# Kernel tuning notes

Hardware: AMD Instinct MI355X
Metric: run time of the kernel (lower is better)

Reference implementation:

```python
import jax, jax.numpy as jnp
import numpy as np

N, C_IN, H, W = 64, 8, 256, 256
E = 4      # edge_emb_dim
D = 4      # node_emb_dim
K = 3      # kernel_size
DN = ('NCHW', 'OIHW', 'NCHW')


def conv2d(x, w, b, padding):
    y = jax.lax.conv_general_dilated(x, w, (1, 1), padding, dimension_numbers=DN)
    return y + b[None, :, None, None]


def _w(key, shape):
    fan_in = shape[1] * shape[2] * shape[3]
    return jax.random.normal(key, shape, dtype=jnp.float32) / np.sqrt(fan_in)


def setup_inputs() -> dict:
    key = jax.random.key(0)
    ks = jax.random.split(key, 16)
    return {
        'x': jax.random.normal(ks[0], (N, C_IN, H, W), dtype=jnp.float32),
        # downsampling: 1x1 conv C_IN -> E (kernel=stride=downsampling_factor=1)
        'w_down': _w(ks[1], (E, C_IN, 1, 1)), 'b_down': jnp.zeros((E,), jnp.float32),
        # edge network phi: two conv3x3 (E->E) each followed by silu
        'w_e1': _w(ks[2], (E, E, K, K)), 'b_e1': jnp.zeros((E,), jnp.float32),
        'w_e2': _w(ks[3], (E, E, K, K)), 'b_e2': jnp.zeros((E,), jnp.float32),
        # upsampling: ConvTranspose with kernel=stride=1 == 1x1 conv E -> E
        'w_up': _w(ks[4], (E, E, 1, 1)), 'b_up': jnp.zeros((E,), jnp.float32),
        # node network psi: conv3x3 (C_IN+E -> D), silu, conv3x3 (D -> D)
        'w_n1': _w(ks[5], (D, C_IN + E, K, K)), 'b_n1': jnp.zeros((D,), jnp.float32),
        'w_n2': _w(ks[6], (D, D, K, K)), 'b_n2': jnp.zeros((D,), jnp.float32),
        # pre_resid: 1x1 conv C_IN -> D (since in_channels != node_emb_dim)
        'w_r': _w(ks[7], (D, C_IN, 1, 1)), 'b_r': jnp.zeros((D,), jnp.float32),
    }


def reference(x, w_down, b_down, w_e1, b_e1, w_e2, b_e2, w_up, b_up,
              w_n1, b_n1, w_n2, b_n2, w_r, b_r):
    # vmap(downsampling)(x): treat cell axis N as conv batch. (N,E,H,W)
    z = conv2d(x, w_down, b_down, 'VALID')
    # cell-wise edge CNN phi
    h = jax.nn.silu(conv2d(z, w_e1, b_e1, 'SAME'))
    h = jax.nn.silu(conv2d(h, w_e2, b_e2, 'SAME'))
    # sum-aggregate over cells -> A: (E,H,W)
    A = h.sum(axis=0)
    # upsampling (kernel=stride=1 transpose conv == 1x1 conv); pad is a no-op here
    A = conv2d(A[None], w_up, b_up, 'VALID')[0]
    # node update: concat [x, A] on channels, cell-interaction CNN psi
    y = jnp.concatenate([x, jnp.broadcast_to(A[None], (N, E, H, W))], axis=1)
    y = jax.nn.silu(conv2d(y, w_n1, b_n1, 'SAME'))
    y = conv2d(y, w_n2, b_n2, 'SAME')
    # residual with channel-matching 1x1 conv
    y = y + conv2d(x, w_r, b_r, 'VALID')
    return y
```

## Files before the change

### kernel.cpp

```cpp
#include <hip/hip_runtime.h>
#include <hip/hip_bf16.h>

#define NCELL 64
#define CIN 8
#define EE 4
#define DD 4
#define HH 256
#define WW 256

#define EBH 32
#define NBH 26
#define NBANDS_E (HH / EBH)
#define NBANDS_N ((HH + NBH - 1) / NBH)
#define NSTRIP 5

__device__ __forceinline__ float4 f4z() { return make_float4(0.f, 0.f, 0.f, 0.f); }
__device__ __forceinline__ float silu1(float v) { return v / (1.0f + __expf(-v)); }
__device__ __forceinline__ float4 silu4f(const float a[4]) {
    return make_float4(silu1(a[0]), silu1(a[1]), silu1(a[2]), silu1(a[3]));
}
__device__ __forceinline__ float4 shfL(float4 v) {
    return make_float4(__shfl_up(v.x, 1), __shfl_up(v.y, 1),
                       __shfl_up(v.z, 1), __shfl_up(v.w, 1));
}
__device__ __forceinline__ float4 shfR(float4 v) {
    return make_float4(__shfl_down(v.x, 1), __shfl_down(v.y, 1),
                       __shfl_down(v.z, 1), __shfl_down(v.w, 1));
}

#define COMP(v,i) ((i)==0?(v).x:(i)==1?(v).y:(i)==2?(v).z:(v).w)

__device__ __forceinline__ void conv_group(const float4* L, const float4* C, const float4* R,
                                           const float* __restrict__ w, int ostride, int ibase,
                                           float acc[4]) {
#pragma unroll
    for (int dy = 0; dy < 3; ++dy) {
#pragma unroll
        for (int ci = 0; ci < 4; ++ci) {
            const float aL = COMP(L[dy], ci);
            const float aC = COMP(C[dy], ci);
            const float aR = COMP(R[dy], ci);
#pragma unroll
            for (int o = 0; o < 4; ++o) {
                const int base = o * ostride + (ibase + ci) * 9 + dy * 3;
                acc[o] = fmaf(aL, w[base + 0], acc[o]);
                acc[o] = fmaf(aC, w[base + 1], acc[o]);
                acc[o] = fmaf(aR, w[base + 2], acc[o]);
            }
        }
    }
}

__global__ __launch_bounds__(256) void edge_kernel(
    const float* __restrict__ x,
    const float* __restrict__ w_down, const float* __restrict__ b_down,
    const float* __restrict__ w_e1, const float* __restrict__ b_e1,
    const float* __restrict__ w_e2, const float* __restrict__ b_e2,
    float4* __restrict__ P)
{
    const int lane = threadIdx.x & 63;
    const int wv = threadIdx.x >> 6;
    const int y0 = blockIdx.x * EBH;
    const int s = blockIdx.y;
    const int n = blockIdx.z * 4 + wv;
    const int cx = s * 60 + lane - 2;
    const bool colok = (unsigned)cx < (unsigned)WW;
    const bool payload = (lane >= 2) && (lane < 62) && colok;
    const float* __restrict__ xn = x + (size_t)n * CIN * HH * WW;

    const float bd0 = b_down[0], bd1 = b_down[1], bd2 = b_down[2], bd3 = b_down[3];
    const float be10 = b_e1[0], be11 = b_e1[1], be12 = b_e1[2], be13 = b_e1[3];
    const float be20 = b_e2[0], be21 = b_e2[1], be22 = b_e2[2], be23 = b_e2[3];

    float4 za0 = f4z(), za1 = f4z(), za2 = f4z();
    float4 zb0 = f4z(), zb1 = f4z(), zb2 = f4z();
    float4 zc0 = f4z(), zc1 = f4z(), zc2 = f4z();
    float4 ha0 = f4z(), ha1 = f4z(), ha2 = f4z();
    float4 hb0 = f4z(), hb1 = f4z(), hb2 = f4z();
    float4 hc0 = f4z(), hc1 = f4z(), hc2 = f4z();

    for (int k = 0; k < EBH + 4; ++k) {
        const int zr = y0 - 2 + k;

        float4 zn = f4z();
        if ((unsigned)zr < (unsigned)HH) {
            if (colok) {
                float a0 = bd0, a1 = bd1, a2 = bd2, a3 = bd3;
#pragma unroll
                for (int i = 0; i < CIN; ++i) {
                    const float xv = xn[((size_t)i * HH + zr) * WW + cx];
                    a0 = fmaf(xv, w_down[0 * CIN + i], a0);
                    a1 = fmaf(xv, w_down[1 * CIN + i], a1);
                    a2 = fmaf(xv, w_down[2 * CIN + i], a2);
                    a3 = fmaf(xv, w_down[3 * CIN + i], a3);
                }
                zn = make_float4(a0, a1, a2, a3);
            }
        }
        za0 = za1; za1 = za2; za2 = zn;
        zb0 = zb1; zb1 = zb2; zb2 = shfL(zn);
        zc0 = zc1; zc1 = zc2; zc2 = shfR(zn);

        if (k >= 2) {
            float acc[4] = { be10, be11, be12, be13 };
            {
                float4 L[3] = { zb0, zb1, zb2 };
                float4 C[3] = { za0, za1, za2 };
                float4 R[3] = { zc0, zc1, zc2 };
                conv_group(L, C, R, w_e1, 36, 0, acc);
            }
            const int hr = zr - 1;
            const float4 hn = ((unsigned)hr < (unsigned)HH && colok) ? silu4f(acc) : f4z();
            ha0 = ha1; ha1 = ha2; ha2 = hn;
            hb0 = hb1; hb1 = hb2; hb2 = shfL(hn);
            hc0 = hc1; hc1 = hc2; hc2 = shfR(hn);
        }

        if (k >= 4) {
            float acc[4] = { be20, be21, be22, be23 };
            {
                float4 L[3] = { hb0, hb1, hb2 };
                float4 C[3] = { ha0, ha1, ha2 };
                float4 R[3] = { hc0, hc1, hc2 };
                conv_group(L, C, R, w_e2, 36, 0, acc);
            }
            if (payload) {
                const int orow = zr - 2;
                P[(size_t)n * (HH * WW) + orow * WW + cx] = silu4f(acc);
            }
        }
    }
}

__global__ __launch_bounds__(256) void reduce_kernel(
    const float4* __restrict__ P, float4* __restrict__ A4)
{
    const int p = blockIdx.x * 256 + threadIdx.x;
    float4 a = f4z(), b = f4z(), c = f4z(), d = f4z();
#pragma unroll
    for (int nn = 0; nn < NCELL; nn += 4) {
        const float4 v0 = P[(size_t)(nn + 0) * (HH * WW) + p];
        const float4 v1 = P[(size_t)(nn + 1) * (HH * WW) + p];
        const float4 v2 = P[(size_t)(nn + 2) * (HH * WW) + p];
        const float4 v3 = P[(size_t)(nn + 3) * (HH * WW) + p];
        a.x += v0.x; a.y += v0.y; a.z += v0.z; a.w += v0.w;
        b.x += v1.x; b.y += v1.y; b.z += v1.z; b.w += v1.w;
        c.x += v2.x; c.y += v2.y; c.z += v2.z; c.w += v2.w;
        d.x += v3.x; d.y += v3.y; d.z += v3.z; d.w += v3.w;
    }
    A4[p] = make_float4(a.x + b.x + c.x + d.x, a.y + b.y + c.y + d.y,
                        a.z + b.z + c.z + d.z, a.w + b.w + c.w + d.w);
}

__global__ __launch_bounds__(256) void node_kernel(
    const float* __restrict__ x, const float* __restrict__ A,
    const float* __restrict__ w_up, const float* __restrict__ b_up,
    const float* __restrict__ w_n1, const float* __restrict__ b_n1,
    const float* __restrict__ w_n2, const float* __restrict__ b_n2,
    const float* __restrict__ w_r, const float* __restrict__ b_r,
    float* __restrict__ out)
{
    const int lane = threadIdx.x & 63;
    const int wv = threadIdx.x >> 6;
    const int y0 = blockIdx.x * NBH;
    const int h = min(NBH, HH - y0);
    const int s = blockIdx.y;
    const int n = blockIdx.z * 4 + wv;
    const int cx = s * 60 + lane - 2;
    const bool colok = (unsigned)cx < (unsigned)WW;
    const bool payload = (lane >= 2) && (lane < 62) && colok;
    const float* __restrict__ xn = x + (size_t)n * CIN * HH * WW;
    const float4* __restrict__ A4 = reinterpret_cast<const float4*>(A);

    const float bu0 = b_up[0], bu1 = b_up[1], bu2 = b_up[2], bu3 = b_up[3];
    const float bn10 = b_n1[0], bn11 = b_n1[1], bn12 = b_n1[2], bn13 = b_n1[3];
    const float br0 = b_n2[0] + b_r[0], br1 = b_n2[1] + b_r[1];
    const float br2 = b_n2[2] + b_r[2], br3 = b_n2[3] + b_r[3];

    float4 sa[3][3];
#pragma unroll
    for (int g = 0; g < 3; ++g) { sa[g][0] = f4z(); sa[g][1] = f4z(); sa[g][2] = f4z(); }
    float4 ya[3] = { f4z(), f4z(), f4z() };
    float4 yb[3] = { f4z(), f4z(), f4z() };
    float4 yc[3] = { f4z(), f4z(), f4z() };

    for (int k = 0; k < h + 4; ++k) {
        const int zr = y0 - 2 + k;

        float4 Sn0 = f4z(), Sn1 = f4z(), Sn2 = f4z();
        if ((unsigned)zr < (unsigned)HH) {
            if (colok) {
                float xv[CIN];
#pragma unroll
                for (int i = 0; i < CIN; ++i) xv[i] = xn[((size_t)i * HH + zr) * WW + cx];
                Sn0 = make_float4(xv[0], xv[1], xv[2], xv[3]);
                Sn1 = make_float4(xv[4], xv[5], xv[6], xv[7]);
                const float4 a4 = A4[zr * WW + cx];
                float u0 = bu0, u1 = bu1, u2 = bu2, u3 = bu3;
#pragma unroll
                for (int e = 0; e < 4; ++e) {
                    const float av = COMP(a4, e);
                    u0 = fmaf(av, w_up[0 * EE + e], u0);
                    u1 = fmaf(av, w_up[1 * EE + e], u1);
                    u2 = fmaf(av, w_up[2 * EE + e], u2);
                    u3 = fmaf(av, w_up[3 * EE + e], u3);
                }
                Sn2 = make_float4(u0, u1, u2, u3);
            }
        }
        sa[0][0] = sa[0][1]; sa[0][1] = sa[0][2]; sa[0][2] = Sn0;
        sa[1][0] = sa[1][1]; sa[1][1] = sa[1][2]; sa[1][2] = Sn1;
        sa[2][0] = sa[2][1]; sa[2][1] = sa[2][2]; sa[2][2] = Sn2;

        if (k >= 2) {
            float acc[4] = { bn10, bn11, bn12, bn13 };
#pragma unroll
            for (int g = 0; g < 3; ++g) {
                float4 L[3] = { shfL(sa[g][0]), shfL(sa[g][1]), shfL(sa[g][2]) };
                float4 R[3] = { shfR(sa[g][0]), shfR(sa[g][1]), shfR(sa[g][2]) };
                conv_group(L, sa[g], R, w_n1, 108, 4 * g, acc);
            }
            const int hr = zr - 1;
            const float4 yn = ((unsigned)hr < (unsigned)HH && colok) ? silu4f(acc) : f4z();
            ya[0] = ya[1]; ya[1] = ya[2]; ya[2] = yn;
            yb[0] = yb[1]; yb[1] = yb[2]; yb[2] = shfL(yn);
            yc[0] = yc[1]; yc[1] = yc[2]; yc[2] = shfR(yn);
        }

        if (k >= 4) {
            float acc[4] = { br0, br1, br2, br3 };
            conv_group(yb, ya, yc, w_n2, 36, 0, acc);
#pragma unroll
            for (int g = 0; g < 2; ++g) {
                const float4 xr = (g == 0) ? sa[0][0] : sa[1][0];
#pragma unroll
                for (int ci = 0; ci < 4; ++ci) {
                    const float a = COMP(xr, ci);
                    acc[0] = fmaf(a, w_r[0 * CIN + g * 4 + ci], acc[0]);
                    acc[1] = fmaf(a, w_r[1 * CIN + g * 4 + ci], acc[1]);
                    acc[2] = fmaf(a, w_r[2 * CIN + g * 4 + ci], acc[2]);
                    acc[3] = fmaf(a, w_r[3 * CIN + g * 4 + ci], acc[3]);
                }
            }
            if (payload) {
                const int orow = zr - 2;
#pragma unroll
                for (int o = 0; o < 4; ++o)
                    out[(((size_t)n * DD + o) * HH + orow) * WW + cx] = acc[o];
            }
        }
    }
}

extern "C" void kernel_launch(void* const* d_in, const int* in_sizes, int n_in,
                              void* d_out, int out_size, void* d_ws, size_t ws_size,
                              hipStream_t stream) {
    const float* x      = (const float*)d_in[0];
    const float* w_down = (const float*)d_in[1];
    const float* b_down = (const float*)d_in[2];
    const float* w_e1   = (const float*)d_in[3];
    const float* b_e1   = (const float*)d_in[4];
    const float* w_e2   = (const float*)d_in[5];
    const float* b_e2   = (const float*)d_in[6];
    const float* w_up   = (const float*)d_in[7];
    const float* b_up   = (const float*)d_in[8];
    const float* w_n1   = (const float*)d_in[9];
    const float* b_n1   = (const float*)d_in[10];
    const float* w_n2   = (const float*)d_in[11];
    const float* b_n2   = (const float*)d_in[12];
    const float* w_r    = (const float*)d_in[13];
    const float* b_r    = (const float*)d_in[14];
    float* out = (float*)d_out;

    float4* P = (float4*)d_out;
    float* A  = (float*)d_ws;

    edge_kernel<<<dim3(NBANDS_E, NSTRIP, NCELL / 4), dim3(256), 0, stream>>>(
        x, w_down, b_down, w_e1, b_e1, w_e2, b_e2, P);

    reduce_kernel<<<dim3(HH * WW / 256), dim3(256), 0, stream>>>(P, (float4*)A);

    node_kernel<<<dim3(NBANDS_N, NSTRIP, NCELL / 4), dim3(256), 0, stream>>>(
        x, A, w_up, b_up, w_n1, b_n1, w_n2, b_n2, w_r, b_r, out);
}
```

Measured before the change: 311.5 us.

## Move weights into constant memory, halve band heights, split reduce across cells

A prep kernel repacks all conv weights and biases into a __constant__ buffer laid out as output-channel float4 vectors, so each kernel reads weights with vector constant loads instead of scattered scalar global loads. Row-band heights drop from 32/26 to 16/13, giving more blocks and more parallelism at the cost of more halo recomputation. The reduction kernel now splits the 64-cell sum across four waves and combines them through shared memory, which gives four times more blocks. The change adds an extra kernel launch and a hipGetSymbolAddress call on every invocation.

```diff
diff --git a/kernel.cpp b/kernel.cpp
--- a/kernel.cpp
+++ b/kernel.cpp
@@ -8,16 +8,31 @@
 #define HH 256
 #define WW 256
 
-#define EBH 32
-#define NBH 26
+#define EBH 16
+#define NBH 13
 #define NBANDS_E (HH / EBH)
 #define NBANDS_N ((HH + NBH - 1) / NBH)
 #define NSTRIP 5
 
+#define DOWN4 0
+#define E14   8
+#define E24   44
+#define UP4   80
+#define N14   84
+#define N24   192
+#define R4    228
+#define B4    236
+#define CW4_TOTAL 242
+
+__constant__ __align__(16) float CW[CW4_TOTAL * 4];
+
+#define CWF4(i) (reinterpret_cast<const float4*>(CW)[(i)])
+#define COMP(v,i) ((i)==0?(v).x:(i)==1?(v).y:(i)==2?(v).z:(v).w)
+
 __device__ __forceinline__ float4 f4z() { return make_float4(0.f, 0.f, 0.f, 0.f); }
 __device__ __forceinline__ float silu1(float v) { return v / (1.0f + __expf(-v)); }
-__device__ __forceinline__ float4 silu4f(const float a[4]) {
-    return make_float4(silu1(a[0]), silu1(a[1]), silu1(a[2]), silu1(a[3]));
+__device__ __forceinline__ float4 silu4(float4 v) {
+    return make_float4(silu1(v.x), silu1(v.y), silu1(v.z), silu1(v.w));
 }
 __device__ __forceinline__ float4 shfL(float4 v) {
     return make_float4(__shfl_up(v.x, 1), __shfl_up(v.y, 1),
@@ -27,36 +42,58 @@
     return make_float4(__shfl_down(v.x, 1), __shfl_down(v.y, 1),
                        __shfl_down(v.z, 1), __shfl_down(v.w, 1));
 }
-
-#define COMP(v,i) ((i)==0?(v).x:(i)==1?(v).y:(i)==2?(v).z:(v).w)
+__device__ __forceinline__ void fma4(float4& a, float s, float4 w) {
+    a.x = fmaf(s, w.x, a.x);
+    a.y = fmaf(s, w.y, a.y);
+    a.z = fmaf(s, w.z, a.z);
+    a.w = fmaf(s, w.w, a.w);
+}
 
 __device__ __forceinline__ void conv_group(const float4* L, const float4* C, const float4* R,
-                                           const float* __restrict__ w, int ostride, int ibase,
-                                           float acc[4]) {
+                                           int base4, float4& acc) {
 #pragma unroll
     for (int dy = 0; dy < 3; ++dy) {
 #pragma unroll
         for (int ci = 0; ci < 4; ++ci) {
-            const float aL = COMP(L[dy], ci);
-            const float aC = COMP(C[dy], ci);
-            const float aR = COMP(R[dy], ci);
-#pragma unroll
-            for (int o = 0; o < 4; ++o) {
-                const int base = o * ostride + (ibase + ci) * 9 + dy * 3;
-                acc[o] = fmaf(aL, w[base + 0], acc[o]);
-                acc[o] = fmaf(aC, w[base + 1], acc[o]);
-                acc[o] = fmaf(aR, w[base + 2], acc[o]);
-            }
-        }
+            const int b = base4 + ci * 9 + dy * 3;
+            fma4(acc, COMP(L[dy], ci), CWF4(b + 0));
+            fma4(acc, COMP(C[dy], ci), CWF4(b + 1));
+            fma4(acc, COMP(R[dy], ci), CWF4(b + 2));
+        }
+    }
+}
+
+__global__ __launch_bounds__(128) void prep_kernel(
+    const float* __restrict__ wd, const float* __restrict__ bd,
+    const float* __restrict__ we1, const float* __restrict__ be1,
+    const float* __restrict__ we2, const float* __restrict__ be2,
+    const float* __restrict__ wu, const float* __restrict__ bu,
+    const float* __restrict__ wn1, const float* __restrict__ bn1,
+    const float* __restrict__ wn2, const float* __restrict__ bn2,
+    const float* __restrict__ wr, const float* __restrict__ br,
+    float4* __restrict__ cw)
+{
+    const int t = threadIdx.x;
+    if (t < 8)   cw[DOWN4 + t] = make_float4(wd[t], wd[8 + t], wd[16 + t], wd[24 + t]);
+    if (t < 36)  cw[E14 + t]   = make_float4(we1[t], we1[36 + t], we1[72 + t], we1[108 + t]);
+    if (t < 36)  cw[E24 + t]   = make_float4(we2[t], we2[36 + t], we2[72 + t], we2[108 + t]);
+    if (t < 4)   cw[UP4 + t]   = make_float4(wu[t], wu[4 + t], wu[8 + t], wu[12 + t]);
+    if (t < 108) cw[N14 + t]   = make_float4(wn1[t], wn1[108 + t], wn1[216 + t], wn1[324 + t]);
+    if (t < 36)  cw[N24 + t]   = make_float4(wn2[t], wn2[36 + t], wn2[72 + t], wn2[108 + t]);
+    if (t < 8)   cw[R4 + t]    = make_float4(wr[t], wr[8 + t], wr[16 + t], wr[24 + t]);
+    if (t == 0) {
+        cw[B4 + 0] = make_float4(bd[0], bd[1], bd[2], bd[3]);
+        cw[B4 + 1] = make_float4(be1[0], be1[1], be1[2], be1[3]);
+        cw[B4 + 2] = make_float4(be2[0], be2[1], be2[2], be2[3]);
+        cw[B4 + 3] = make_float4(bu[0], bu[1], bu[2], bu[3]);
+        cw[B4 + 4] = make_float4(bn1[0], bn1[1], bn1[2], bn1[3]);
+        cw[B4 + 5] = make_float4(bn2[0] + br[0], bn2[1] + br[1],
+                                 bn2[2] + br[2], bn2[3] + br[3]);
     }
 }
 
 __global__ __launch_bounds__(256) void edge_kernel(
-    const float* __restrict__ x,
-    const float* __restrict__ w_down, const float* __restrict__ b_down,
-    const float* __restrict__ w_e1, const float* __restrict__ b_e1,
-    const float* __restrict__ w_e2, const float* __restrict__ b_e2,
-    float4* __restrict__ P)
+    const float* __restrict__ x, float4* __restrict__ P)
 {
     const int lane = threadIdx.x & 63;
     const int wv = threadIdx.x >> 6;
@@ -68,9 +105,9 @@
     const bool payload = (lane >= 2) && (lane < 62) && colok;
     const float* __restrict__ xn = x + (size_t)n * CIN * HH * WW;
 
-    const float bd0 = b_down[0], bd1 = b_down[1], bd2 = b_down[2], bd3 = b_down[3];
-    const float be10 = b_e1[0], be11 = b_e1[1], be12 = b_e1[2], be13 = b_e1[3];
-    const float be20 = b_e2[0], be21 = b_e2[1], be22 = b_e2[2], be23 = b_e2[3];
+    const float4 bdn = CWF4(B4 + 0);
+    const float4 be1 = CWF4(B4 + 1);
+    const float4 be2 = CWF4(B4 + 2);
 
     float4 za0 = f4z(), za1 = f4z(), za2 = f4z();
     float4 zb0 = f4z(), zb1 = f4z(), zb2 = f4z();
@@ -83,50 +120,42 @@
         const int zr = y0 - 2 + k;
 
         float4 zn = f4z();
-        if ((unsigned)zr < (unsigned)HH) {
-            if (colok) {
-                float a0 = bd0, a1 = bd1, a2 = bd2, a3 = bd3;
-#pragma unroll
-                for (int i = 0; i < CIN; ++i) {
-                    const float xv = xn[((size_t)i * HH + zr) * WW + cx];
-                    a0 = fmaf(xv, w_down[0 * CIN + i], a0);
-                    a1 = fmaf(xv, w_down[1 * CIN + i], a1);
-                    a2 = fmaf(xv, w_down[2 * CIN + i], a2);
-                    a3 = fmaf(xv, w_down[3 * CIN + i], a3);
-                }
-                zn = make_float4(a0, a1, a2, a3);
-            }
+        if ((unsigned)zr < (unsigned)HH && colok) {
+            zn = bdn;
+#pragma unroll
+            for (int i = 0; i < CIN; ++i)
+                fma4(zn, xn[((size_t)i * HH + zr) * WW + cx], CWF4(DOWN4 + i));
         }
         za0 = za1; za1 = za2; za2 = zn;
         zb0 = zb1; zb1 = zb2; zb2 = shfL(zn);
         zc0 = zc1; zc1 = zc2; zc2 = shfR(zn);
 
         if (k >= 2) {
-            float acc[4] = { be10, be11, be12, be13 };
+            float4 acc = be1;
             {
                 float4 L[3] = { zb0, zb1, zb2 };
                 float4 C[3] = { za0, za1, za2 };
                 float4 R[3] = { zc0, zc1, zc2 };
-                conv_group(L, C, R, w_e1, 36, 0, acc);
+                conv_group(L, C, R, E14, acc);
             }
             const int hr = zr - 1;
-            const float4 hn = ((unsigned)hr < (unsigned)HH && colok) ? silu4f(acc) : f4z();
+            const float4 hn = ((unsigned)hr < (unsigned)HH && colok) ? silu4(acc) : f4z();
             ha0 = ha1; ha1 = ha2; ha2 = hn;
             hb0 = hb1; hb1 = hb2; hb2 = shfL(hn);
             hc0 = hc1; hc1 = hc2; hc2 = shfR(hn);
         }
 
         if (k >= 4) {
-            float acc[4] = { be20, be21, be22, be23 };
+            float4 acc = be2;
             {
                 float4 L[3] = { hb0, hb1, hb2 };
                 float4 C[3] = { ha0, ha1, ha2 };
                 float4 R[3] = { hc0, hc1, hc2 };
-                conv_group(L, C, R, w_e2, 36, 0, acc);
+                conv_group(L, C, R, E24, acc);
             }
             if (payload) {
                 const int orow = zr - 2;
-                P[(size_t)n * (HH * WW) + orow * WW + cx] = silu4f(acc);
+                P[(size_t)n * (HH * WW) + orow * WW + cx] = silu4(acc);
             }
         }
     }
@@ -135,29 +164,30 @@
 __global__ __launch_bounds__(256) void reduce_kernel(
     const float4* __restrict__ P, float4* __restrict__ A4)
 {
-    const int p = blockIdx.x * 256 + threadIdx.x;
-    float4 a = f4z(), b = f4z(), c = f4z(), d = f4z();
-#pragma unroll
-    for (int nn = 0; nn < NCELL; nn += 4) {
-        const float4 v0 = P[(size_t)(nn + 0) * (HH * WW) + p];
-        const float4 v1 = P[(size_t)(nn + 1) * (HH * WW) + p];
-        const float4 v2 = P[(size_t)(nn + 2) * (HH * WW) + p];
-        const float4 v3 = P[(size_t)(nn + 3) * (HH * WW) + p];
+    __shared__ float4 buf[256];
+    const int tid = threadIdx.x;
+    const int pix = blockIdx.x * 64 + (tid & 63);
+    const int c0 = (tid >> 6) * 16;
+    float4 a = f4z(), b = f4z();
+#pragma unroll
+    for (int j = 0; j < 16; j += 2) {
+        const float4 v0 = P[(size_t)(c0 + j + 0) * (HH * WW) + pix];
+        const float4 v1 = P[(size_t)(c0 + j + 1) * (HH * WW) + pix];
         a.x += v0.x; a.y += v0.y; a.z += v0.z; a.w += v0.w;
         b.x += v1.x; b.y += v1.y; b.z += v1.z; b.w += v1.w;
-        c.x += v2.x; c.y += v2.y; c.z += v2.z; c.w += v2.w;
-        d.x += v3.x; d.y += v3.y; d.z += v3.z; d.w += v3.w;
-    }
-    A4[p] = make_float4(a.x + b.x + c.x + d.x, a.y + b.y + c.y + d.y,
-                        a.z + b.z + c.z + d.z, a.w + b.w + c.w + d.w);
+    }
+    buf[tid] = make_float4(a.x + b.x, a.y + b.y, a.z + b.z, a.w + b.w);
+    __syncthreads();
+    if (tid < 64) {
+        const float4 p0 = buf[tid], p1 = buf[tid + 64], p2 = buf[tid + 128], p3 = buf[tid + 192];
+        A4[blockIdx.x * 64 + tid] =
+            make_float4(p0.x + p1.x + p2.x + p3.x, p0.y + p1.y + p2.y + p3.y,
+                        p0.z + p1.z + p2.z + p3.z, p0.w + p1.w + p2.w + p3.w);
+    }
 }
 
 __global__ __launch_bounds__(256) void node_kernel(
     const float* __restrict__ x, const float* __restrict__ A,
-    const float* __restrict__ w_up, const float* __restrict__ b_up,
-    const float* __restrict__ w_n1, const float* __restrict__ b_n1,
-    const float* __restrict__ w_n2, const float* __restrict__ b_n2,
-    const float* __restrict__ w_r, const float* __restrict__ b_r,
     float* __restrict__ out)
 {
     const int lane = threadIdx.x & 63;
@@ -172,10 +202,9 @@
     const float* __restrict__ xn = x + (size_t)n * CIN * HH * WW;
     const float4* __restrict__ A4 = reinterpret_cast<const float4*>(A);
 
-    const float bu0 = b_up[0], bu1 = b_up[1], bu2 = b_up[2], bu3 = b_up[3];
-    const float bn10 = b_n1[0], bn11 = b_n1[1], bn12 = b_n1[2], bn13 = b_n1[3];
-    const float br0 = b_n2[0] + b_r[0], br1 = b_n2[1] + b_r[1];
-    const float br2 = b_n2[2] + b_r[2], br3 = b_n2[3] + b_r[3];
+    const float4 bup = CWF4(B4 + 3);
+    const float4 bn1 = CWF4(B4 + 4);
+    const float4 bn2r = CWF4(B4 + 5);
 
     float4 sa[3][3];
 #pragma unroll
@@ -188,65 +217,51 @@
         const int zr = y0 - 2 + k;
 
         float4 Sn0 = f4z(), Sn1 = f4z(), Sn2 = f4z();
-        if ((unsigned)zr < (unsigned)HH) {
-            if (colok) {
-                float xv[CIN];
-#pragma unroll
-                for (int i = 0; i < CIN; ++i) xv[i] = xn[((size_t)i * HH + zr) * WW + cx];
-                Sn0 = make_float4(xv[0], xv[1], xv[2], xv[3]);
-                Sn1 = make_float4(xv[4], xv[5], xv[6], xv[7]);
-                const float4 a4 = A4[zr * WW + cx];
-                float u0 = bu0, u1 = bu1, u2 = bu2, u3 = bu3;
-#pragma unroll
-                for (int e = 0; e < 4; ++e) {
-                    const float av = COMP(a4, e);
-                    u0 = fmaf(av, w_up[0 * EE + e], u0);
-                    u1 = fmaf(av, w_up[1 * EE + e], u1);
-                    u2 = fmaf(av, w_up[2 * EE + e], u2);
-                    u3 = fmaf(av, w_up[3 * EE + e], u3);
-                }
-                Sn2 = make_float4(u0, u1, u2, u3);
-            }
+        if ((unsigned)zr < (unsigned)HH && colok) {
+            float xv[CIN];
+#pragma unroll
+            for (int i = 0; i < CIN; ++i) xv[i] = xn[((size_t)i * HH + zr) * WW + cx];
+            Sn0 = make_float4(xv[0], xv[1], xv[2], xv[3]);
+            Sn1 = make_float4(xv[4], xv[5], xv[6], xv[7]);
+            const float4 a4 = A4[zr * WW + cx];
+            Sn2 = bup;
+#pragma unroll
+            for (int e = 0; e < 4; ++e)
+                fma4(Sn2, COMP(a4, e), CWF4(UP4 + e));
         }
         sa[0][0] = sa[0][1]; sa[0][1] = sa[0][2]; sa[0][2] = Sn0;
         sa[1][0] = sa[1][1]; sa[1][1] = sa[1][2]; sa[1][2] = Sn1;
         sa[2][0] = sa[2][1]; sa[2][1] = sa[2][2]; sa[2][2] = Sn2;
 
         if (k >= 2) {
-            float acc[4] = { bn10, bn11, bn12, bn13 };
+            float4 acc = bn1;
 #pragma unroll
             for (int g = 0; g < 3; ++g) {
                 float4 L[3] = { shfL(sa[g][0]), shfL(sa[g][1]), shfL(sa[g][2]) };
                 float4 R[3] = { shfR(sa[g][0]), shfR(sa[g][1]), shfR(sa[g][2]) };
-                conv_group(L, sa[g], R, w_n1, 108, 4 * g, acc);
+                conv_group(L, sa[g], R, N14 + g * 36, acc);
             }
             const int hr = zr - 1;
-            const float4 yn = ((unsigned)hr < (unsigned)HH && colok) ? silu4f(acc) : f4z();
+            const float4 yn = ((unsigned)hr < (unsigned)HH && colok) ? silu4(acc) : f4z();
             ya[0] = ya[1]; ya[1] = ya[2]; ya[2] = yn;
             yb[0] = yb[1]; yb[1] = yb[2]; yb[2] = shfL(yn);
             yc[0] = yc[1]; yc[1] = yc[2]; yc[2] = shfR(yn);
         }
 
         if (k >= 4) {
-            float acc[4] = { br0, br1, br2, br3 };
-            conv_group(yb, ya, yc, w_n2, 36, 0, acc);
-#pragma unroll
-            for (int g = 0; g < 2; ++g) {
-                const float4 xr = (g == 0) ? sa[0][0] : sa[1][0];
-#pragma unroll
-                for (int ci = 0; ci < 4; ++ci) {
-                    const float a = COMP(xr, ci);
-                    acc[0] = fmaf(a, w_r[0 * CIN + g * 4 + ci], acc[0]);
-                    acc[1] = fmaf(a, w_r[1 * CIN + g * 4 + ci], acc[1]);
-                    acc[2] = fmaf(a, w_r[2 * CIN + g * 4 + ci], acc[2]);
-                    acc[3] = fmaf(a, w_r[3 * CIN + g * 4 + ci], acc[3]);
-                }
+            float4 acc = bn2r;
+            conv_group(yb, ya, yc, N24, acc);
+#pragma unroll
+            for (int ci = 0; ci < 4; ++ci) {
+                fma4(acc, COMP(sa[0][0], ci), CWF4(R4 + ci));
+                fma4(acc, COMP(sa[1][0], ci), CWF4(R4 + 4 + ci));
             }
             if (payload) {
                 const int orow = zr - 2;
-#pragma unroll
-                for (int o = 0; o < 4; ++o)
-                    out[(((size_t)n * DD + o) * HH + orow) * WW + cx] = acc[o];
+                out[(((size_t)n * DD + 0) * HH + orow) * WW + cx] = acc.x;
+                out[(((size_t)n * DD + 1) * HH + orow) * WW + cx] = acc.y;
+                out[(((size_t)n * DD + 2) * HH + orow) * WW + cx] = acc.z;
+                out[(((size_t)n * DD + 3) * HH + orow) * WW + cx] = acc.w;
             }
         }
     }
@@ -275,11 +290,16 @@
     float4* P = (float4*)d_out;
     float* A  = (float*)d_ws;
 
-    edge_kernel<<<dim3(NBANDS_E, NSTRIP, NCELL / 4), dim3(256), 0, stream>>>(
-        x, w_down, b_down, w_e1, b_e1, w_e2, b_e2, P);
-
-    reduce_kernel<<<dim3(HH * WW / 256), dim3(256), 0, stream>>>(P, (float4*)A);
-
-    node_kernel<<<dim3(NBANDS_N, NSTRIP, NCELL / 4), dim3(256), 0, stream>>>(
-        x, A, w_up, b_up, w_n1, b_n1, w_n2, b_n2, w_r, b_r, out);
-}
+    void* cwp = nullptr;
+    (void)hipGetSymbolAddress(&cwp, HIP_SYMBOL(CW));
+
+    prep_kernel<<<dim3(1), dim3(128), 0, stream>>>(
+        w_down, b_down, w_e1, b_e1, w_e2, b_e2, w_up, b_up,
+        w_n1, b_n1, w_n2, b_n2, w_r, b_r, (float4*)cwp);
+
+    edge_kernel<<<dim3(NBANDS_E, NSTRIP, NCELL / 4), dim3(256), 0, stream>>>(x, P);
+
+    reduce_kernel<<<dim3(HH * WW / 64), dim3(256), 0, stream>>>(P, (float4*)A);
+
+    node_kernel<<<dim3(NBANDS_N, NSTRIP, NCELL / 4), dim3(256), 0, stream>>>(x, A, out);
+}
```

New measurement: 938.0 us. 201% more time.
